# Kernel optimization log

Measured on AMD Instinct MI355X. Metric: run time of the kernel, lower is better.

## Reference

```python
import jax, jax.numpy as jnp
import numpy as np
import math

B, D, OUT = 512, 128, 100000
S, M = 32.0, 0.5
COS_M, SIN_M = math.cos(M), math.sin(M)
TH = math.cos(math.pi - M)
MM = math.sin(math.pi - M) * M
M1 = M2 = M3 = M5 = 1.0


def setup_inputs() -> dict:
    key = jax.random.key(0)
    k1, k2, k3, k4, k5, k6 = jax.random.split(key, 6)
    x = jax.random.normal(k1, (B, D), dtype=jnp.float32)
    label = jax.random.randint(k2, (B,), 0, OUT)
    k = jax.random.uniform(k3, (1, 1, 1024, 1024), dtype=jnp.float32)
    x0 = jax.random.uniform(k4, (1, 3, 112, 96), dtype=jnp.float32)
    img = jax.random.uniform(k5, (1, 3, 112, 96), dtype=jnp.float32)
    # xavier_uniform for [OUT, D]
    limit = math.sqrt(6.0 / (OUT + D))
    W = jax.random.uniform(k6, (OUT, D), minval=-limit, maxval=limit, dtype=jnp.float32)
    return {"x": x, "label": label, "k": k, "x0": x0, "img": img, "W": W}


def _arcmargin(x, W, label):
    xn = x / jnp.linalg.norm(x, axis=-1, keepdims=True)
    wn = W / jnp.linalg.norm(W, axis=-1, keepdims=True)
    cosine = xn @ wn.T                                  # [B, OUT]
    sine = jnp.sqrt(jnp.clip(1.0 - cosine * cosine, 0.0))
    phi = cosine * COS_M - sine * SIN_M
    phi = jnp.where(cosine - TH > 0, phi, cosine - MM)   # easy_margin=False
    one_hot = jax.nn.one_hot(label, OUT, dtype=cosine.dtype)
    logits = S * (one_hot * phi + (1.0 - one_hot) * cosine)
    logp = jax.nn.log_softmax(logits, axis=-1)
    return -jnp.mean(jnp.take_along_axis(logp, label[:, None], axis=1))


def _tv_loss(k):
    h, w = k.shape[-2], k.shape[-1]
    count_h = (h - 1) * w
    count_w = h * (w - 1)
    h_tv = jnp.sum((k[:, :, 1:, :] - k[:, :, :-1, :]) ** 2)
    w_tv = jnp.sum((k[:, :, :, 1:] - k[:, :, :, :-1]) ** 2)
    return -1.0 * 2.0 * (h_tv / count_h + w_tv / count_w)  # weight = -1*loss_weight


def _bin_loss(k):
    # sum over pixels of k^2 + (k-1)^2, / (h*w), then mean over batch/channel
    return jnp.mean(k * k + (k - 1.0) ** 2)


def _inv_loss(k):
    k = jax.lax.stop_gradient(k)  # original detaches before numpy FFT
    mag = jnp.abs(jnp.fft.fftn(k, axes=(-2, -1)))
    return jnp.mean(jnp.sum(mag, axis=(-1, -2)))  # L1 norm over (-1,-2), then mean


def reference(x, label, k, x0, img, W):
    loss = (M1 * _arcmargin(x, W, label)
            + M2 * _tv_loss(k)
            + M3 * _bin_loss(k)
            + M5 * _inv_loss(k))
    return loss
```

## Files before the change

### kernel.cpp

```cpp
#include <hip/hip_runtime.h>


typedef short bf16x8 __attribute__((ext_vector_type(8)));
typedef float f32x4 __attribute__((ext_vector_type(4)));
typedef unsigned short u16;
typedef unsigned int u32;

#define BATCH 512
#define DIM 128
#define OUTN 100000
#define OUTPAD 100096
#define NOBLK 782
#define GEMMBLK 3128
#define NROW2 1564
#define CHUNKS 16
#define CHSZ2 98
#define SSCALE 32.0f
#define K2C 46.166241308446828f
#define COSM 0.8775825618903728f
#define SINM 0.479425538604203f
#define THC (-0.8775825618903728f)
#define MMC 0.2397127693021015f

#define S1_FFT 1024
#define S1_TV  2048
#define S1_XP  2176
#define S1_NW  27200

__device__ inline u16 f2bf(float f) {
  union { float f; u32 u; } v; v.f = f;
  u32 r = v.u + 0x7FFFu + ((v.u >> 16) & 1u);
  return (u16)(r >> 16);
}

__device__ inline float waveRedSum(float v) {
#pragma unroll
  for (int off = 1; off < 64; off <<= 1) v += __shfl_xor(v, off, 64);
  return v;
}

__global__ __launch_bounds__(256) void stage1_k(const float* __restrict__ x,
                                                const float* __restrict__ W,
                                                const int* __restrict__ label,
                                                const float* __restrict__ kimg,
                                                u32* __restrict__ xh,
                                                float* __restrict__ coslab,
                                                u32* __restrict__ Wh,
                                                float4* __restrict__ tvpart,
                                                float2* __restrict__ fbuf) {
  __shared__ __align__(16) float smem[2064];
  int t = threadIdx.x;
  int bid = blockIdx.x;

  if (bid < S1_FFT) {
    float* re = smem;
    float* im = smem + 1024;
    int r = bid;
#pragma unroll
    for (int i = 0; i < 4; i++) {
      int idx = i * 256 + t;
      re[idx] = kimg[r * 1024 + idx];
      im[idx] = 0.f;
    }
    __syncthreads();
    for (int lh = 9; lh >= 0; lh--) {
      int hlf = 1 << lh;
      float ang = -6.283185307179586f / (float)(hlf * 2);
#pragma unroll
      for (int i = 0; i < 2; i++) {
        int bf = i * 256 + t;
        int pos = bf & (hlf - 1);
        int g = bf >> lh;
        int i0 = (g << (lh + 1)) + pos;
        int i1 = i0 + hlf;
        float ur = re[i0], ui = im[i0], vr = re[i1], vi = im[i1];
        float s, c;
        __sincosf(ang * (float)pos, &s, &c);
        re[i0] = ur + vr; im[i0] = ui + vi;
        float dr = ur - vr, di = ui - vi;
        re[i1] = dr * c - di * s;
        im[i1] = dr * s + di * c;
      }
      __syncthreads();
    }
#pragma unroll
    for (int i = 0; i < 4; i++) {
      int idx = i * 256 + t;
      fbuf[(size_t)r * 1024 + idx] = make_float2(re[idx], im[idx]);
    }
  } else if (bid < S1_TV) {
    int r = bid - S1_FFT;
    int idx = r * 1024 + t * 4;
    float4 v = *(const float4*)&kimg[idx];
    float bs = v.x * v.x + (v.x - 1.f) * (v.x - 1.f)
             + v.y * v.y + (v.y - 1.f) * (v.y - 1.f)
             + v.z * v.z + (v.z - 1.f) * (v.z - 1.f)
             + v.w * v.w + (v.w - 1.f) * (v.w - 1.f);
    float d0 = v.y - v.x, d1 = v.z - v.y, d2 = v.w - v.z;
    float wsm = d0 * d0 + d1 * d1 + d2 * d2;
    if (t < 255) { float e4 = kimg[idx + 4]; float d3 = e4 - v.w; wsm += d3 * d3; }
    float hs = 0.f;
    if (r < 1023) {
      float4 n = *(const float4*)&kimg[idx + 1024];
      float h0 = n.x - v.x, h1 = n.y - v.y, h2 = n.z - v.z, h3 = n.w - v.w;
      hs = h0 * h0 + h1 * h1 + h2 * h2 + h3 * h3;
    }
    hs = waveRedSum(hs); wsm = waveRedSum(wsm); bs = waveRedSum(bs);
    float (*red)[4] = (float(*)[4])smem;
    if ((t & 63) == 0) { int w = t >> 6; red[0][w] = hs; red[1][w] = wsm; red[2][w] = bs; }
    __syncthreads();
    if (t == 0)
      tvpart[r] = make_float4(red[0][0] + red[0][1] + red[0][2] + red[0][3],
                              red[1][0] + red[1][1] + red[1][2] + red[1][3],
                              red[2][0] + red[2][1] + red[2][2] + red[2][3], 0.f);
  } else if (bid < S1_XP) {
    int b = (bid - S1_TV) * 4 + (t >> 6);
    int lane = t & 63;
    size_t xb = (size_t)b * DIM;
    float2 v = *(const float2*)&x[xb + lane * 2];
    int lab = label[b];
    size_t wb = (size_t)lab * DIM;
    float2 w = *(const float2*)&W[wb + lane * 2];
    float ss = waveRedSum(v.x * v.x + v.y * v.y);
    float d  = waveRedSum(v.x * w.x + v.y * w.y);
    float nw = waveRedSum(w.x * w.x + w.y * w.y);
    float inv = rsqrtf(ss);
    xh[b * 64 + lane] = (u32)f2bf(v.x * inv) | ((u32)f2bf(v.y * inv) << 16);
    if (lane == 0) coslab[b] = d * rsqrtf(ss * nw);
  } else {
    int row = (bid - S1_XP) * 4 + (t >> 6);
    int lane = t & 63;
    size_t base = (size_t)row * DIM;
    if (row < OUTN) {
      float2 v = *(const float2*)&W[base + lane * 2];
      float ss = waveRedSum(v.x * v.x + v.y * v.y);
      float inv = rsqrtf(ss);
      Wh[row * 64 + lane] = (u32)f2bf(v.x * inv) | ((u32)f2bf(v.y * inv) << 16);
    } else {
      Wh[row * 64 + lane] = 0;
    }
  }
}

__global__ __launch_bounds__(256, 4) void stage2_k(const u16* __restrict__ Wh,
                                                   const u16* __restrict__ xh,
                                                   float* __restrict__ gpart,
                                                   const float2* __restrict__ fbuf,
                                                   float* __restrict__ fftpart) {
  __shared__ __align__(16) char smem[32784];
  int t = threadIdx.x;
  int bid = blockIdx.x;

  if (bid < GEMMBLK) {
    int o = bid >> 2, bt = bid & 3;
    int o0 = o * 128, b0 = bt * 128;
    u16* Ash = (u16*)smem;
    u16* Bsh = (u16*)(smem + 16384);
    int wv = t >> 6, lane = t & 63;
    int wo = (wv & 1) << 6, wbs = (wv >> 1) << 6;
    int m16 = lane & 15, q = lane >> 4;
    f32x4 acc[4][4] = {};

#pragma unroll
    for (int kc = 0; kc < 2; kc++) {
      if (kc) __syncthreads();
#pragma unroll
      for (int i = 0; i < 4; i++) {
        int f = i * 256 + t;
        int rr = f >> 3, gg = f & 7;
        int sw = ((gg ^ (rr & 7)) * 8);
        *(uint4*)&Ash[rr * 64 + sw] =
            *(const uint4*)&Wh[(size_t)(o0 + rr) * DIM + kc * 64 + gg * 8];
        *(uint4*)&Bsh[rr * 64 + sw] =
            *(const uint4*)&xh[(size_t)(b0 + rr) * DIM + kc * 64 + gg * 8];
      }
      __syncthreads();
#pragma unroll
      for (int kk = 0; kk < 2; kk++) {
        bf16x8 af[4], bfr[4];
#pragma unroll
        for (int i = 0; i < 4; i++) {
          int row = wo + i * 16 + m16;
          af[i] = *(const bf16x8*)&Ash[row * 64 + (((kk * 4 + q) ^ (row & 7)) * 8)];
        }
#pragma unroll
        for (int j = 0; j < 4; j++) {
          int row = wbs + j * 16 + m16;
          bfr[j] = *(const bf16x8*)&Bsh[row * 64 + (((kk * 4 + q) ^ (row & 7)) * 8)];
        }
#pragma unroll
        for (int i = 0; i < 4; i++)
#pragma unroll
          for (int j = 0; j < 4; j++)
            acc[i][j] = __builtin_amdgcn_mfma_f32_16x16x32_bf16(af[i], bfr[j], acc[i][j], 0, 0, 0);
      }
    }
#pragma unroll
    for (int j = 0; j < 4; j++) {
      float s = 0.f;
#pragma unroll
      for (int i = 0; i < 4; i++)
#pragma unroll
        for (int r = 0; r < 4; r++)
          s += exp2f(K2C * acc[i][j][r]);
      s += __shfl_xor(s, 16, 64);
      s += __shfl_xor(s, 32, 64);
      if (q == 0)
        gpart[(size_t)(o * 2 + (wv & 1)) * 512 + b0 + wbs + j * 16 + m16] = s;
    }
  } else {
    float2* arr = (float2*)smem;
    float* red = (float*)(smem + 32768);
    int c0 = (bid - GEMMBLK) * 4;
#pragma unroll
    for (int i = 0; i < 16; i++) {
      int li = i * 256 + t;
      int rr = li >> 2, c = li & 3;
      arr[rr * 4 + c] = fbuf[(size_t)rr * 1024 + c0 + c];
    }
    __syncthreads();
    for (int lh = 9; lh >= 0; lh--) {
      int hlf = 1 << lh;
      float ang = -6.283185307179586f / (float)(hlf * 2);
#pragma unroll
      for (int i = 0; i < 8; i++) {
        int w = i * 256 + t;
        int c = w & 3, bf = w >> 2;
        int pos = bf & (hlf - 1), g2i = bf >> lh;
        int i0 = ((g2i << (lh + 1)) + pos) * 4 + c;
        int i1 = i0 + hlf * 4;
        float2 u = arr[i0], v = arr[i1];
        float s, cc;
        __sincosf(ang * (float)pos, &s, &cc);
        arr[i0] = make_float2(u.x + v.x, u.y + v.y);
        float dr = u.x - v.x, di = u.y - v.y;
        arr[i1] = make_float2(dr * cc - di * s, dr * s + di * cc);
      }
      __syncthreads();
    }
    float s = 0.f;
#pragma unroll
    for (int i = 0; i < 16; i++) {
      float2 v = arr[i * 256 + t];
      s += sqrtf(v.x * v.x + v.y * v.y);
    }
    s = waveRedSum(s);
    if ((t & 63) == 0) red[t >> 6] = s;
    __syncthreads();
    if (t == 0) fftpart[bid - GEMMBLK] = red[0] + red[1] + red[2] + red[3];
  }
}

__global__ __launch_bounds__(256) void gemmred_k(const float* __restrict__ gpart,
                                                 float* __restrict__ g2,
                                                 const u32* __restrict__ xh32,
                                                 const u32* __restrict__ Wh32,
                                                 const int* __restrict__ label,
                                                 float* __restrict__ labexp) {
  int t = threadIdx.x;
  int blk = blockIdx.x;
  if (blk < 32) {
    int chunk = blk >> 1, half = blk & 1;
    int b = half * 256 + t;
    int rBeg = chunk * CHSZ2;
    int rEnd = rBeg + CHSZ2; if (rEnd > NROW2) rEnd = NROW2;
    float s = 0.f;
    for (int r = rBeg; r < rEnd; r++) s += gpart[(size_t)r * 512 + b];
    g2[chunk * 512 + b] = s;
  } else {
    int b = (blk - 32) * 256 + t;
    int lab = label[b];
    const u32* xr = &xh32[b * 64];
    const u32* wr = &Wh32[(size_t)lab * 64];
    float d = 0.f;
#pragma unroll 8
    for (int i = 0; i < 64; i++) {
      u32 xa = xr[i], wa = wr[i];
      float xl = __uint_as_float(xa << 16), xhp = __uint_as_float(xa & 0xFFFF0000u);
      float wl = __uint_as_float(wa << 16), whp = __uint_as_float(wa & 0xFFFF0000u);
      d += xl * wl + xhp * whp;
    }
    labexp[b] = exp2f(K2C * d);
  }
}

__global__ __launch_bounds__(256) void final_k(const float* __restrict__ coslab,
                                               const float* __restrict__ g2,
                                               const float4* __restrict__ tvpart,
                                               const float* __restrict__ fftpart,
                                               const float* __restrict__ labexp,
                                               float* __restrict__ out) {
  int t = threadIdx.x;
  float arc = 0.f, hs = 0.f, wsm = 0.f, bs = 0.f, fs = 0.f;
#pragma unroll
  for (int i = 0; i < 2; i++) {
    int b = i * 256 + t;
    float se = 0.f;
#pragma unroll
    for (int c = 0; c < CHUNKS; c++) se += g2[c * 512 + b];
    se -= 96.0f;
    se -= labexp[b];
    float cl = coslab[b];
    float sine = sqrtf(fmaxf(0.f, 1.f - cl * cl));
    float phi = cl * COSM - sine * SINM;
    if (!(cl - THC > 0.f)) phi = cl - MMC;
    arc += __logf(se + exp2f(K2C * phi)) - SSCALE * phi;
  }
#pragma unroll
  for (int i = 0; i < 4; i++) {
    float4 p = tvpart[i * 256 + t];
    hs += p.x; wsm += p.y; bs += p.z;
  }
  fs = fftpart[t];
  arc = waveRedSum(arc); hs = waveRedSum(hs); wsm = waveRedSum(wsm);
  bs = waveRedSum(bs); fs = waveRedSum(fs);
  __shared__ float red[5][4];
  if ((t & 63) == 0) {
    int w = t >> 6;
    red[0][w] = arc; red[1][w] = hs; red[2][w] = wsm; red[3][w] = bs; red[4][w] = fs;
  }
  __syncthreads();
  if (t == 0) {
    float A = 0, H = 0, Wv = 0, Bv = 0, F = 0;
#pragma unroll
    for (int w = 0; w < 4; w++) {
      A += red[0][w]; H += red[1][w]; Wv += red[2][w]; Bv += red[3][w]; F += red[4][w];
    }
    float cnt = 1023.0f * 1024.0f;
    out[0] = A * (1.0f / 512.0f) - 2.0f * (H / cnt + Wv / cnt)
           + Bv * (1.0f / 1048576.0f) + F;
  }
}

extern "C" void kernel_launch(void* const* d_in, const int* in_sizes, int n_in,
                              void* d_out, int out_size, void* d_ws, size_t ws_size,
                              hipStream_t stream) {
  const float* x = (const float*)d_in[0];
  const int* label = (const int*)d_in[1];
  const float* kimg = (const float*)d_in[2];
  const float* W = (const float*)d_in[5];
  float* out = (float*)d_out;
  char* ws = (char*)d_ws;
  float*  coslab  = (float*)(ws + 0);
  u32*    xh      = (u32*)(ws + 2048);
  u32*    Wh      = (u32*)(ws + 133120);
  float2* fbuf    = (float2*)(ws + 25757696);
  float*  gpart   = (float*)(ws + 34146304);
  float*  g2      = (float*)(ws + 35350528);
  float4* tvpart  = (float4*)(ws + 35383296);
  float*  fftpart = (float*)(ws + 35399680);
  float*  labexp  = (float*)(ws + 35400704);

  hipLaunchKernelGGL(stage1_k, dim3(S1_NW), dim3(256), 0, stream,
                     x, W, label, kimg, xh, coslab, Wh, tvpart, fbuf);
  hipLaunchKernelGGL(stage2_k, dim3(GEMMBLK + 256), dim3(256), 0, stream,
                     (const u16*)Wh, (const u16*)xh, gpart, fbuf, fftpart);
  hipLaunchKernelGGL(gemmred_k, dim3(34), dim3(256), 0, stream,
                     gpart, g2, xh, Wh, label, labexp);
  hipLaunchKernelGGL(final_k, dim3(1), dim3(256), 0, stream,
                     coslab, g2, tvpart, fftpart, labexp, out);
}
```

Baseline: 166.3 us.

## Pack two W rows per wave, schedule FFT blocks first, group GEMM tiles

The W normalization now has each wave handle two rows with float4 loads and a half-wave reduction, roughly halving the stage-1 block count. In stage 2 the FFT blocks move to the front of the grid so their long serial work starts early and overlaps the GEMM tiles. GEMM tiles are remapped so that groups of 8 output tiles share all 4 batch tiles, improving L2 reuse of W tiles. Workspace offsets for the later buffers shift, and a few GEMM blocks exit early as padding.

New measurement: 159.7 us. 1.04x faster.

```diff
diff --git a/kernel.cpp b/kernel.cpp
--- a/kernel.cpp
+++ b/kernel.cpp
@@ -11,7 +11,6 @@
 #define OUTN 100000
 #define OUTPAD 100096
 #define NOBLK 782
-#define GEMMBLK 3128
 #define NROW2 1564
 #define CHUNKS 16
 #define CHSZ2 98
@@ -25,7 +24,10 @@
 #define S1_FFT 1024
 #define S1_TV  2048
 #define S1_XP  2176
-#define S1_NW  27200
+#define S1_NW  14688
+
+#define S2_GEMM0 256
+#define S2_NBLK  3392
 
 __device__ inline u16 f2bf(float f) {
   union { float f; u32 u; } v; v.f = f;
@@ -36,6 +38,12 @@
 __device__ inline float waveRedSum(float v) {
 #pragma unroll
   for (int off = 1; off < 64; off <<= 1) v += __shfl_xor(v, off, 64);
+  return v;
+}
+
+__device__ inline float halfRedSum(float v) {
+#pragma unroll
+  for (int off = 1; off < 32; off <<= 1) v += __shfl_xor(v, off, 64);
   return v;
 }
 
@@ -128,17 +136,18 @@
     xh[b * 64 + lane] = (u32)f2bf(v.x * inv) | ((u32)f2bf(v.y * inv) << 16);
     if (lane == 0) coslab[b] = d * rsqrtf(ss * nw);
   } else {
-    int row = (bid - S1_XP) * 4 + (t >> 6);
+    int p = (bid - S1_XP) * 4 + (t >> 6);
     int lane = t & 63;
-    size_t base = (size_t)row * DIM;
-    if (row < OUTN) {
-      float2 v = *(const float2*)&W[base + lane * 2];
-      float ss = waveRedSum(v.x * v.x + v.y * v.y);
-      float inv = rsqrtf(ss);
-      Wh[row * 64 + lane] = (u32)f2bf(v.x * inv) | ((u32)f2bf(v.y * inv) << 16);
-    } else {
-      Wh[row * 64 + lane] = 0;
-    }
+    if (2 * p >= OUTN) {
+      *(uint2*)&Wh[(size_t)p * 128 + lane * 2] = make_uint2(0u, 0u);
+      return;
+    }
+    float4 v = *(const float4*)&W[(size_t)p * 256 + lane * 4];
+    float ss = halfRedSum(v.x * v.x + v.y * v.y + v.z * v.z + v.w * v.w);
+    float inv = rsqrtf(ss);
+    u32 lo = (u32)f2bf(v.x * inv) | ((u32)f2bf(v.y * inv) << 16);
+    u32 hi = (u32)f2bf(v.z * inv) | ((u32)f2bf(v.w * inv) << 16);
+    *(uint2*)&Wh[(size_t)p * 128 + lane * 2] = make_uint2(lo, hi);
   }
 }
 
@@ -151,8 +160,10 @@
   int t = threadIdx.x;
   int bid = blockIdx.x;
 
-  if (bid < GEMMBLK) {
-    int o = bid >> 2, bt = bid & 3;
+  if (bid >= S2_GEMM0) {
+    int wgrp = (bid - S2_GEMM0) & 31, g = (bid - S2_GEMM0) >> 5;
+    int o = g * 8 + (wgrp & 7), bt = wgrp >> 3;
+    if (o >= NOBLK) return;
     int o0 = o * 128, b0 = bt * 128;
     u16* Ash = (u16*)smem;
     u16* Bsh = (u16*)(smem + 16384);
@@ -211,7 +222,7 @@
   } else {
     float2* arr = (float2*)smem;
     float* red = (float*)(smem + 32768);
-    int c0 = (bid - GEMMBLK) * 4;
+    int c0 = bid * 4;
 #pragma unroll
     for (int i = 0; i < 16; i++) {
       int li = i * 256 + t;
@@ -247,7 +258,7 @@
     s = waveRedSum(s);
     if ((t & 63) == 0) red[t >> 6] = s;
     __syncthreads();
-    if (t == 0) fftpart[bid - GEMMBLK] = red[0] + red[1] + red[2] + red[3];
+    if (t == 0) fftpart[bid] = red[0] + red[1] + red[2] + red[3];
   }
 }
 
@@ -346,14 +357,14 @@
   u32*    Wh      = (u32*)(ws + 133120);
   float2* fbuf    = (float2*)(ws + 25757696);
   float*  gpart   = (float*)(ws + 34146304);
-  float*  g2      = (float*)(ws + 35350528);
-  float4* tvpart  = (float4*)(ws + 35383296);
-  float*  fftpart = (float*)(ws + 35399680);
-  float*  labexp  = (float*)(ws + 35400704);
+  float*  g2      = (float*)(ws + 37349376);
+  float4* tvpart  = (float4*)(ws + 37382144);
+  float*  fftpart = (float*)(ws + 37398528);
+  float*  labexp  = (float*)(ws + 37399552);
 
   hipLaunchKernelGGL(stage1_k, dim3(S1_NW), dim3(256), 0, stream,
                      x, W, label, kimg, xh, coslab, Wh, tvpart, fbuf);
-  hipLaunchKernelGGL(stage2_k, dim3(GEMMBLK + 256), dim3(256), 0, stream,
+  hipLaunchKernelGGL(stage2_k, dim3(S2_NBLK), dim3(256), 0, stream,
                      (const u16*)Wh, (const u16*)xh, gpart, fbuf, fftpart);
   hipLaunchKernelGGL(gemmred_k, dim3(34), dim3(256), 0, stream,
                      gpart, g2, xh, Wh, label, labexp);
```
